# Kernel tuning notes

Measured on AMD Instinct MI355X. Metric: run time of the kernel, lower is better.

Reference implementation:

```python
import jax, jax.numpy as jnp
import numpy as np

NUM_CLASSES = 2
THRESHOLD = 0.35   # overlap_thresh
NEG_POS = 7        # negative:positive mining ratio
VAR0, VAR1 = 0.1, 0.2  # self.variance


def point_form(boxes):
    # (cx,cy,w,h) -> (xmin,ymin,xmax,ymax); boxes [P,4]
    return jnp.concatenate([boxes[:, :2] - boxes[:, 2:] / 2,
                            boxes[:, :2] + boxes[:, 2:] / 2], axis=1)


def jaccard(box_a, box_b):
    # box_a [B,O,4] xyxy, box_b [P,4] xyxy -> IoU [B,O,P]
    max_xy = jnp.minimum(box_a[:, :, None, 2:], box_b[None, None, :, 2:])
    min_xy = jnp.maximum(box_a[:, :, None, :2], box_b[None, None, :, :2])
    wh = jnp.clip(max_xy - min_xy, 0.0)
    inter = wh[..., 0] * wh[..., 1]
    area_a = ((box_a[..., 2] - box_a[..., 0]) * (box_a[..., 3] - box_a[..., 1]))[:, :, None]
    area_b = ((box_b[:, 2] - box_b[:, 0]) * (box_b[:, 3] - box_b[:, 1]))[None, None, :]
    return inter / (area_a + area_b - inter)


def encode(matched, priors):
    # matched [B,P,4] xyxy, priors [1,P,4] cxcywh -> offsets [B,P,4]
    g_cxcy = (matched[..., :2] + matched[..., 2:]) / 2 - priors[..., :2]
    g_cxcy = g_cxcy / (VAR0 * priors[..., 2:])
    g_wh = (matched[..., 2:] - matched[..., :2]) / priors[..., 2:]
    g_wh = jnp.log(g_wh) / VAR1
    return jnp.concatenate([g_cxcy, g_wh], axis=-1)


def match(truths, labels, priors):
    # truths [B,O,4] xyxy, labels [B,O] float, priors [P,4] cxcywh
    overlaps = jaccard(truths, point_form(priors))      # [B,O,P]
    best_prior_idx = jnp.argmax(overlaps, axis=2)       # [B,O] best prior per gt
    best_truth_overlap = jnp.max(overlaps, axis=1)      # [B,P]
    best_truth_idx = jnp.argmax(overlaps, axis=1)       # [B,P] best gt per prior
    O = truths.shape[1]

    def fix(bto, bti, bpi):
        # ensure every gt keeps its best prior (index_fill_ / loop in torch)
        bto = bto.at[bpi].set(2.0)
        bti = bti.at[bpi].set(jnp.arange(O))
        return bto, bti

    best_truth_overlap, best_truth_idx = jax.vmap(fix)(
        best_truth_overlap, best_truth_idx, best_prior_idx)
    matched = jnp.take_along_axis(truths, best_truth_idx[..., None], axis=1)  # [B,P,4]
    conf = jnp.take_along_axis(labels, best_truth_idx, axis=1).astype(jnp.int32) + 1
    conf = jnp.where(best_truth_overlap < THRESHOLD, 0, conf)  # background
    loc = encode(matched, priors[None])
    return loc, conf


def setup_inputs() -> dict:
    key = jax.random.key(0)
    k1, k2, k3, k4, k5, k6 = jax.random.split(key, 6)
    B, P, O, C = 32, 32768, 32, NUM_CLASSES
    loc_data = jax.random.normal(k1, (B, P, 4), jnp.float32)
    conf_data = jax.random.normal(k2, (B, P, C), jnp.float32)
    # priors: (cx,cy,w,h) in [0,1], wh in [0.02,0.3]
    p_cxcy = jax.random.uniform(k3, (P, 2), jnp.float32)
    p_wh = 0.02 + 0.28 * jax.random.uniform(k4, (P, 2), jnp.float32)
    priors = jnp.concatenate([p_cxcy, p_wh], axis=1)
    # targets: valid xyxy boxes + label column (label 0 -> class 1 after +1)
    t_cxcy = 0.1 + 0.8 * jax.random.uniform(k5, (B, O, 2), jnp.float32)
    t_wh = 0.05 + 0.2 * jax.random.uniform(k6, (B, O, 2), jnp.float32)
    boxes = jnp.concatenate([t_cxcy - t_wh / 2, t_cxcy + t_wh / 2], axis=2)
    labels = jnp.zeros((B, O, 1), jnp.float32)
    targets = jnp.concatenate([boxes, labels], axis=2)
    return {"loc_data": loc_data, "conf_data": conf_data,
            "priors": priors, "targets": targets}


def reference(loc_data, conf_data, priors, targets):
    B, P, C = conf_data.shape
    truths = targets[..., :4]
    labels = targets[..., 4]
    loc_t, conf_t = match(truths, labels, priors)   # [B,P,4], [B,P] int
    pos = conf_t > 0                                # [B,P]

    # localization: smooth-L1 summed over positives
    diff = loc_data - loc_t
    ad = jnp.abs(diff)
    sl1 = jnp.where(ad < 1.0, 0.5 * diff * diff, ad - 0.5)
    loss_l = jnp.sum(sl1 * pos[..., None].astype(loc_data.dtype))

    # per-prior CE loss for hard-negative mining
    lse = jax.nn.logsumexp(conf_data, axis=2)                            # [B,P]
    picked = jnp.take_along_axis(conf_data, conf_t[..., None], axis=2)[..., 0]
    ce = lse - picked                                                    # [B,P]
    mine = jnp.where(pos, 0.0, ce)
    # double-argsort rank trick (descending)
    loss_idx = jnp.argsort(-mine, axis=1)
    idx_rank = jnp.argsort(loss_idx, axis=1)
    num_pos = jnp.sum(pos, axis=1, keepdims=True)                        # [B,1]
    num_neg = jnp.minimum(NEG_POS * num_pos, P - 1)
    neg = idx_rank < num_neg

    sel = pos | neg
    loss_c = jnp.sum(jnp.where(sel, ce, 0.0))

    N = jnp.maximum(jnp.sum(num_pos).astype(jnp.float32), 1.0)
    return loss_l / N, loss_c / N
```

## Files before the change

### kernel.cpp

```cpp
#include <hip/hip_runtime.h>
#include <stdint.h>

#define NB 32
#define NP 32768
#define NO 32
#define THRESH 0.35f
#define NT1 64

typedef unsigned long long u64;
typedef unsigned int u32;

__device__ __forceinline__ float iou_corners(float px1, float py1, float px2, float py2, float ab,
                                             float tx1, float ty1, float tx2, float ty2, float aa)
{
#pragma clang fp contract(off)
    float iw = fminf(tx2, px2) - fmaxf(tx1, px1);
    float ih = fminf(ty2, py2) - fmaxf(ty1, py1);
    iw = fmaxf(iw, 0.f); ih = fmaxf(ih, 0.f);
    float inter = iw * ih;
    return __fdividef(inter, aa + ab - inter);
}

__device__ __forceinline__ float smooth_l1_sum(float4 ld, float4 pr, float4 tt)
{
#pragma clang fp contract(off)
    float g0 = __fdividef((tt.x + tt.z) * 0.5f - pr.x, 0.1f * pr.z);
    float g1 = __fdividef((tt.y + tt.w) * 0.5f - pr.y, 0.1f * pr.w);
    float g2 = __logf(__fdividef(tt.z - tt.x, pr.z)) * 5.0f;
    float g3 = __logf(__fdividef(tt.w - tt.y, pr.w)) * 5.0f;
    float d0 = ld.x - g0, d1 = ld.y - g1, d2 = ld.z - g2, d3 = ld.w - g3;
    float a0 = fabsf(d0), a1 = fabsf(d1), a2 = fabsf(d2), a3 = fabsf(d3);
    return (a0 < 1.f ? 0.5f * d0 * d0 : a0 - 0.5f)
         + (a1 < 1.f ? 0.5f * d1 * d1 : a1 - 0.5f)
         + (a2 < 1.f ? 0.5f * d2 * d2 : a2 - 0.5f)
         + (a3 < 1.f ? 0.5f * d3 * d3 : a3 - 0.5f);
}

__device__ __forceinline__ float lse2(float c0, float c1)
{
#pragma clang fp contract(off)
    float mm = fmaxf(c0, c1), mn = fminf(c0, c1);
    return mm + __logf(1.f + __expf(mn - mm));
}

__global__ __launch_bounds__(256) void kern1(
        const float* __restrict__ loc, const float* __restrict__ conf,
        const float* __restrict__ priors, const float* __restrict__ targets,
        float* __restrict__ mine, u64* __restrict__ bpk_part,
        float* __restrict__ part_sl1, float* __restrict__ part_cep, int* __restrict__ part_np,
        float* __restrict__ sl_tot, float* __restrict__ c_tot,
        int* __restrict__ np_tot, int* __restrict__ done_cnt)
{
#pragma clang fp contract(off)
    __shared__ __align__(16) float4 tbc[NO];
    __shared__ float ta[NO], tlab[NO];
    __shared__ u64 keys[NO];
    __shared__ float rs0[4], rs1[4];
    __shared__ int rc[4];
    const int b = blockIdx.y, x = blockIdx.x, tid = threadIdx.x;
    if (b == 0 && x == 0 && tid == 0) {
        *sl_tot = 0.f; *c_tot = 0.f; *np_tot = 0; *done_cnt = 0;
    }
    if (tid < NO * 5) {
        int o = tid / 5, c = tid % 5;
        float v = targets[b * NO * 5 + tid];
        if (c < 4) ((float*)&tbc[o])[c] = v; else tlab[o] = v;
    }
    if (tid < NO) keys[tid] = 0ull;
    __syncthreads();
    if (tid < NO) {
        float4 t = tbc[tid];
        ta[tid] = (t.z - t.x) * (t.w - t.y);
    }
    __syncthreads();

    const int p0 = x * 512 + tid * 2;
    float4 pr[2];
    float px1[2], py1[2], px2[2], py2[2], ab[2];
#pragma unroll
    for (int j = 0; j < 2; ++j) {
        pr[j] = ((const float4*)priors)[p0 + j];
        px1[j] = pr[j].x - pr[j].z * 0.5f;
        py1[j] = pr[j].y - pr[j].w * 0.5f;
        px2[j] = pr[j].x + pr[j].z * 0.5f;
        py2[j] = pr[j].y + pr[j].w * 0.5f;
        ab[j]  = pr[j].z * pr[j].w;
    }
    u64 bk[2] = {0ull, 0ull};
    const int lane_o = tid & 31;
    for (int it = 0; it < NO; ++it) {
        const int o = (it + lane_o) & 31;
        float4 tt = tbc[o];
        float aa = ta[o];
        float iou2[2];
#pragma unroll
        for (int j = 0; j < 2; ++j) {
            float iou = iou_corners(px1[j], py1[j], px2[j], py2[j], ab[j],
                                    tt.x, tt.y, tt.z, tt.w, aa);
            iou2[j] = iou;
            u64 ko = ((u64)__float_as_uint(iou) << 6) | (u64)(63 - o);
            bk[j] = bk[j] > ko ? bk[j] : ko;
        }
        float vm = fmaxf(iou2[0], iou2[1]);
        u64 cur = keys[o];
        if (__float_as_uint(vm) > (u32)(cur >> 32)) {
            float bi = iou2[1]; int bp = p0 + 1;
            if (iou2[0] >= bi) { bi = iou2[0]; bp = p0; }
            atomicMax(&keys[o], ((u64)__float_as_uint(bi) << 32) | (u64)(~(u32)bp));
        }
    }

    const size_t gbase = (size_t)b * NP + p0;
    float4 cf = ((const float4*)conf)[gbase >> 1];
    float c0[2] = {cf.x, cf.z};
    float c1[2] = {cf.y, cf.w};
    float2 mout;
    float s_sl1 = 0.f, s_cep = 0.f;
    int np = 0;
#pragma unroll
    for (int j = 0; j < 2; ++j) {
        u32 vb = (u32)(bk[j] >> 6);
        float bv = __uint_as_float(vb);
        int o = 63 - (int)(bk[j] & 63);
        int cfv = (bv < THRESH) ? 0 : ((int)tlab[o] + 1);
        bool pos = cfv > 0;
        float4 ld = ((const float4*)loc)[gbase + j];
        float sl1 = smooth_l1_sum(ld, pr[j], tbc[o]);
        float ce = lse2(c0[j], c1[j]) - ((cfv == 0) ? c0[j] : c1[j]);
        if (pos) { s_sl1 += sl1; s_cep += ce; np++; }
        ((float*)&mout)[j] = pos ? 0.f : ce;
    }
    ((float2*)mine)[gbase >> 1] = mout;

#pragma unroll
    for (int m = 32; m; m >>= 1) {
        s_sl1 += __shfl_xor(s_sl1, m, 64);
        s_cep += __shfl_xor(s_cep, m, 64);
        np    += __shfl_xor(np, m, 64);
    }
    int lane = tid & 63, w = tid >> 6;
    if (lane == 0) { rs0[w] = s_sl1; rs1[w] = s_cep; rc[w] = np; }
    __syncthreads();
    if (tid == 0) {
        float t0 = 0.f, t1 = 0.f; int t2 = 0;
        for (int i = 0; i < 4; ++i) { t0 += rs0[i]; t1 += rs1[i]; t2 += rc[i]; }
        part_sl1[b * NT1 + x] = t0;
        part_cep[b * NT1 + x] = t1;
        part_np [b * NT1 + x] = t2;
    }
    if (tid < NO) bpk_part[(b * NT1 + x) * 32 + tid] = keys[tid];
}

#define HCOL 33
__global__ __launch_bounds__(1024) void kern3(
        const float* __restrict__ loc, const float* __restrict__ conf,
        const float* __restrict__ priors, const float* __restrict__ targets,
        const u64* __restrict__ bpk_part, const float* __restrict__ mine,
        const float* __restrict__ part_sl1, const float* __restrict__ part_cep,
        const int* __restrict__ part_np,
        float* __restrict__ sl_tot, float* __restrict__ c_tot,
        int* __restrict__ np_tot, int* __restrict__ done_cnt,
        float* __restrict__ out)
{
#pragma clang fp contract(off)
    const int b = blockIdx.x, tid = threadIdx.x;
    const int wave = tid >> 6, lane = tid & 63;
    const int cl = lane & 31;
    __shared__ __align__(16) float4 tbc[NO];
    __shared__ float tlab[NO], tas[NO];
    __shared__ u32 pp[NO];
    __shared__ u32 flags[1024];
    __shared__ int hist[256 * HCOL];
    __shared__ int total[256];
    __shared__ float rs[16];
    __shared__ int rc2[16];
    __shared__ float sh_sl1, sh_cep;
    __shared__ int sh_np, sh_k, sh_kk;
    __shared__ u32 sh_prefix;

    if (tid < NO * 5) {
        int o = tid / 5, c = tid % 5;
        float v = targets[b * NO * 5 + tid];
        if (c < 4) ((float*)&tbc[o])[c] = v; else tlab[o] = v;
    }
    flags[tid] = 0u;
    for (int i = tid; i < 256 * HCOL; i += 1024) hist[i] = 0;

    const float* mb = mine + (size_t)b * NP;
    float v[32];
#pragma unroll
    for (int q = 0; q < 8; ++q) {
        float4 t4 = ((const float4*)mb)[q * 1024 + tid];
        v[4 * q] = t4.x; v[4 * q + 1] = t4.y; v[4 * q + 2] = t4.z; v[4 * q + 3] = t4.w;
    }
    __syncthreads();
#pragma unroll 8
    for (int j = 0; j < 32; ++j)
        atomicAdd(&hist[(__float_as_uint(v[j]) >> 24) * HCOL + cl], 1);
    if (tid < NO) {
        float4 t = tbc[tid];
        tas[tid] = (t.z - t.x) * (t.w - t.y);
        u64 key = 0ull;
        for (int xx = 0; xx < NT1; ++xx) {
            u64 t2 = bpk_part[(b * NT1 + xx) * 32 + tid];
            key = t2 > key ? t2 : key;
        }
        pp[tid] = (key >> 32) ? ~(u32)key : 0u;
    }
    __syncthreads();
    if (tid < NO) {
        const int o = tid;
        const u32 p = pp[o];
        float dsl1 = 0.f, dcep = 0.f; int dnp = 0;
        bool last = true;
        for (int o2 = o + 1; o2 < NO; ++o2)
            if (pp[o2] == p) { last = false; break; }
        if (last) {
            float4 prr = ((const float4*)priors)[p];
            float px1 = prr.x - prr.z * 0.5f, py1 = prr.y - prr.w * 0.5f;
            float px2 = prr.x + prr.z * 0.5f, py2 = prr.y + prr.w * 0.5f;
            float ab = prr.z * prr.w;
            float bv = -1.f; int bo_ = 0;
            for (int o2 = 0; o2 < NO; ++o2) {
                float4 t2 = tbc[o2];
                float i2 = iou_corners(px1, py1, px2, py2, ab, t2.x, t2.y, t2.z, t2.w, tas[o2]);
                if (i2 > bv) { bv = i2; bo_ = o2; }
            }
            int cf_pre = (bv < THRESH) ? 0 : ((int)tlab[bo_] + 1);
            size_t gp = (size_t)b * NP + p;
            float4 ld = ((const float4*)loc)[gp];
            float2 c = ((const float2*)conf)[gp];
            float lse = lse2(c.x, c.y);
            int cf_new = (int)tlab[o] + 1;
            dsl1 = smooth_l1_sum(ld, prr, tbc[o]);
            dcep = lse - ((cf_new == 0) ? c.x : c.y);
            dnp = 1;
            if (cf_pre > 0) {
                dsl1 -= smooth_l1_sum(ld, prr, tbc[bo_]);
                dcep -= lse - ((cf_pre == 0) ? c.x : c.y);
                dnp = 0;
            }
            float oldv = mb[p];
            atomicSub(&hist[(__float_as_uint(oldv) >> 24) * HCOL + cl], 1);
            atomicAdd(&hist[cl], 1);
            atomicOr(&flags[p >> 5], 1u << (p & 31));
        }
        float a = part_sl1[b * NT1 + o] + part_sl1[b * NT1 + 32 + o] + dsl1;
        float d = part_cep[b * NT1 + o] + part_cep[b * NT1 + 32 + o] + dcep;
        int   n = part_np [b * NT1 + o] + part_np [b * NT1 + 32 + o] + dnp;
#pragma unroll
        for (int m = 16; m; m >>= 1) {
            a += __shfl_xor(a, m, 32);
            d += __shfl_xor(d, m, 32);
            n += __shfl_xor(n, m, 32);
        }
        if (o == 0) {
            sh_sl1 = a; sh_cep = d; sh_np = n;
            sh_k = min(7 * n, NP - 1); sh_kk = sh_k; sh_prefix = 0u;
        }
    }
    __syncthreads();
#pragma unroll
    for (int q = 0; q < 8; ++q) {
        u32 word = flags[q * 128 + (tid >> 3)];
#pragma unroll
        for (int c = 0; c < 4; ++c)
            if ((word >> (((tid & 7) << 2) + c)) & 1u) v[4 * q + c] = 0.f;
    }
    const int k = sh_k;
    float topk = 0.f;
    if (k > 0) {
        for (int pass = 0; pass < 4; ++pass) {
            if (pass > 0) {
                for (int i = tid; i < 256 * HCOL; i += 1024) hist[i] = 0;
                __syncthreads();
                const int shift = 24 - 8 * pass;
                const u32 pfx = sh_prefix;
#pragma unroll 8
                for (int j = 0; j < 32; ++j) {
                    u32 kb = __float_as_uint(v[j]);
                    if ((u32)(((u64)kb) >> (shift + 8)) == pfx)
                        atomicAdd(&hist[((kb >> shift) & 255) * HCOL + cl], 1);
                }
                __syncthreads();
            }
            if (tid < 512) {
                int bin = tid >> 1;
                const int base = bin * HCOL + (tid & 1) * 16;
                int s = 0;
#pragma unroll
                for (int i = 0; i < 16; ++i) s += hist[base + i];
                s += __shfl_xor(s, 1, 64);
                if ((tid & 1) == 0) total[bin] = s;
            }
            __syncthreads();
            if (tid < 64) {
                int4 h4 = ((const int4*)total)[tid];
                int s3 = h4.w, s2 = h4.z + s3, s1 = h4.y + s2, s0 = h4.x + s1;
                int acc = s0;
#pragma unroll
                for (int off = 1; off < 64; off <<= 1) {
                    int u = __shfl_down(acc, off, 64);
                    if (tid + off < 64) acc += u;
                }
                int excl = acc - s0;
                int kk = sh_kk;
                int cand = -1, nkk = 0;
                if (excl + s3 >= kk)      { cand = 4 * tid + 3; nkk = kk - excl; }
                else if (excl + s2 >= kk) { cand = 4 * tid + 2; nkk = kk - excl - s3; }
                else if (excl + s1 >= kk) { cand = 4 * tid + 1; nkk = kk - excl - s2; }
                else if (excl + s0 >= kk) { cand = 4 * tid + 0; nkk = kk - excl - s1; }
                int cmax = cand;
#pragma unroll
                for (int off = 1; off < 64; off <<= 1) cmax = max(cmax, __shfl_xor(cmax, off, 64));
                if (cand >= 0 && cand == cmax) {
                    sh_prefix = (sh_prefix << 8) | (u32)(cand & 255);
                    sh_kk = nkk;
                }
            }
            __syncthreads();
        }
        const u32 T = sh_prefix;
        const float tval = __uint_as_float(T);
        float s = 0.f; int c2 = 0;
#pragma unroll
        for (int j = 0; j < 32; ++j) {
            if (__float_as_uint(v[j]) > T) { s += v[j]; c2++; }
        }
#pragma unroll
        for (int m = 32; m; m >>= 1) {
            s  += __shfl_xor(s, m, 64);
            c2 += __shfl_xor(c2, m, 64);
        }
        if (lane == 0) { rs[wave] = s; rc2[wave] = c2; }
        __syncthreads();
        if (tid == 0) {
            float st = 0.f; int ct = 0;
            for (int i = 0; i < 16; ++i) { st += rs[i]; ct += rc2[i]; }
            topk = st + (float)(k - ct) * tval;
        }
    }
    if (tid == 0) {
        atomicAdd(sl_tot, sh_sl1);
        atomicAdd(c_tot, sh_cep + topk);
        atomicAdd(np_tot, sh_np);
        __threadfence();
        int d = atomicAdd(done_cnt, 1);
        if (d == NB - 1) {
            float sl = atomicAdd(sl_tot, 0.f);
            float cc = atomicAdd(c_tot, 0.f);
            int   np = atomicAdd(np_tot, 0);
            float N = fmaxf((float)np, 1.f);
            out[0] = sl / N;
            out[1] = cc / N;
        }
    }
}

extern "C" void kernel_launch(void* const* d_in, const int* in_sizes, int n_in,
                              void* d_out, int out_size, void* d_ws, size_t ws_size,
                              hipStream_t stream) {
    const float* loc     = (const float*)d_in[0];
    const float* conf    = (const float*)d_in[1];
    const float* priors  = (const float*)d_in[2];
    const float* targets = (const float*)d_in[3];
    float* out = (float*)d_out;

    char* ws = (char*)d_ws;
    float* mine     = (float*)ws;
    u64*   bpk_part = (u64*)(ws + 4194304);
    float* part_sl1 = (float*)(ws + 4718592);
    float* part_cep = (float*)(ws + 4726784);
    int*   part_np  = (int*)(ws + 4734976);
    float* sl_tot   = (float*)(ws + 4743168);
    float* c_tot    = (float*)(ws + 4743172);
    int*   np_tot   = (int*)(ws + 4743176);
    int*   done_cnt = (int*)(ws + 4743180);

    dim3 g1(NT1, NB);
    kern1<<<g1, 256, 0, stream>>>(loc, conf, priors, targets, mine, bpk_part,
                                  part_sl1, part_cep, part_np,
                                  sl_tot, c_tot, np_tot, done_cnt);
    kern3<<<NB, 1024, 0, stream>>>(loc, conf, priors, targets, bpk_part, mine,
                                   part_sl1, part_cep, part_np,
                                   sl_tot, c_tot, np_tot, done_cnt, out);
}
```

Measured before the change: 127.4 us.

## Replace 4-pass 8-bit radix select with 3-pass 13/13/6-bit histogram select

The per-batch top-k threshold search used four 8-bit radix passes over replicated 256x33 histograms. It now uses three passes with wider digits (13, 13 and 6 bits) over plain 8192-bin shared histograms, found with a block-wide suffix scan. This cuts the number of passes and block barriers. In exchange, the single-copy histograms suffer more atomic contention, and each scan now reads more bins.

```diff
diff --git a/kernel.cpp b/kernel.cpp
--- a/kernel.cpp
+++ b/kernel.cpp
@@ -6,6 +6,7 @@
 #define NO 32
 #define THRESH 0.35f
 #define NT1 64
+#define HB 8192
 
 typedef unsigned long long u64;
 typedef unsigned int u32;
@@ -151,7 +152,6 @@
     if (tid < NO) bpk_part[(b * NT1 + x) * 32 + tid] = keys[tid];
 }
 
-#define HCOL 33
 __global__ __launch_bounds__(1024) void kern3(
         const float* __restrict__ loc, const float* __restrict__ conf,
         const float* __restrict__ priors, const float* __restrict__ targets,
@@ -165,18 +165,18 @@
 #pragma clang fp contract(off)
     const int b = blockIdx.x, tid = threadIdx.x;
     const int wave = tid >> 6, lane = tid & 63;
-    const int cl = lane & 31;
     __shared__ __align__(16) float4 tbc[NO];
     __shared__ float tlab[NO], tas[NO];
     __shared__ u32 pp[NO];
     __shared__ u32 flags[1024];
-    __shared__ int hist[256 * HCOL];
-    __shared__ int total[256];
+    __shared__ int histA[HB], histB[HB];
+    __shared__ int wtot[16];
     __shared__ float rs[16];
     __shared__ int rc2[16];
     __shared__ float sh_sl1, sh_cep;
-    __shared__ int sh_np, sh_k, sh_kk;
-    __shared__ u32 sh_prefix;
+    __shared__ int sh_np, sh_k, sh_kk0, sh_kk1, sh_kk2;
+    __shared__ int sh_pA, sh_pB;
+    __shared__ u32 sh_T;
 
     if (tid < NO * 5) {
         int o = tid / 5, c = tid % 5;
@@ -184,8 +184,11 @@
         if (c < 4) ((float*)&tbc[o])[c] = v; else tlab[o] = v;
     }
     flags[tid] = 0u;
-    for (int i = tid; i < 256 * HCOL; i += 1024) hist[i] = 0;
-
+#pragma unroll
+    for (int i = 0; i < HB / 1024; ++i) {
+        histA[tid + 1024 * i] = 0;
+        histB[tid + 1024 * i] = 0;
+    }
     const float* mb = mine + (size_t)b * NP;
     float v[32];
 #pragma unroll
@@ -194,9 +197,10 @@
         v[4 * q] = t4.x; v[4 * q + 1] = t4.y; v[4 * q + 2] = t4.z; v[4 * q + 3] = t4.w;
     }
     __syncthreads();
+
 #pragma unroll 8
     for (int j = 0; j < 32; ++j)
-        atomicAdd(&hist[(__float_as_uint(v[j]) >> 24) * HCOL + cl], 1);
+        atomicAdd(&histA[__float_as_uint(v[j]) >> 19], 1);
     if (tid < NO) {
         float4 t = tbc[tid];
         tas[tid] = (t.z - t.x) * (t.w - t.y);
@@ -208,6 +212,7 @@
         pp[tid] = (key >> 32) ? ~(u32)key : 0u;
     }
     __syncthreads();
+
     if (tid < NO) {
         const int o = tid;
         const u32 p = pp[o];
@@ -241,8 +246,8 @@
                 dnp = 0;
             }
             float oldv = mb[p];
-            atomicSub(&hist[(__float_as_uint(oldv) >> 24) * HCOL + cl], 1);
-            atomicAdd(&hist[cl], 1);
+            atomicSub(&histA[__float_as_uint(oldv) >> 19], 1);
+            atomicAdd(&histA[0], 1);
             atomicOr(&flags[p >> 5], 1u << (p & 31));
         }
         float a = part_sl1[b * NT1 + o] + part_sl1[b * NT1 + 32 + o] + dsl1;
@@ -256,83 +261,116 @@
         }
         if (o == 0) {
             sh_sl1 = a; sh_cep = d; sh_np = n;
-            sh_k = min(7 * n, NP - 1); sh_kk = sh_k; sh_prefix = 0u;
-        }
-    }
-    __syncthreads();
-#pragma unroll
-    for (int q = 0; q < 8; ++q) {
-        u32 word = flags[q * 128 + (tid >> 3)];
-#pragma unroll
-        for (int c = 0; c < 4; ++c)
-            if ((word >> (((tid & 7) << 2) + c)) & 1u) v[4 * q + c] = 0.f;
-    }
+            sh_k = min(7 * n, NP - 1); sh_kk0 = sh_k;
+        }
+    }
+    __syncthreads();
+
     const int k = sh_k;
+    const int base = tid << 3;
     float topk = 0.f;
     if (k > 0) {
-        for (int pass = 0; pass < 4; ++pass) {
-            if (pass > 0) {
-                for (int i = tid; i < 256 * HCOL; i += 1024) hist[i] = 0;
-                __syncthreads();
-                const int shift = 24 - 8 * pass;
-                const u32 pfx = sh_prefix;
-#pragma unroll 8
-                for (int j = 0; j < 32; ++j) {
-                    u32 kb = __float_as_uint(v[j]);
-                    if ((u32)(((u64)kb) >> (shift + 8)) == pfx)
-                        atomicAdd(&hist[((kb >> shift) & 255) * HCOL + cl], 1);
-                }
-                __syncthreads();
-            }
-            if (tid < 512) {
-                int bin = tid >> 1;
-                const int base = bin * HCOL + (tid & 1) * 16;
-                int s = 0;
-#pragma unroll
-                for (int i = 0; i < 16; ++i) s += hist[base + i];
-                s += __shfl_xor(s, 1, 64);
-                if ((tid & 1) == 0) total[bin] = s;
-            }
-            __syncthreads();
-            if (tid < 64) {
-                int4 h4 = ((const int4*)total)[tid];
-                int s3 = h4.w, s2 = h4.z + s3, s1 = h4.y + s2, s0 = h4.x + s1;
-                int acc = s0;
-#pragma unroll
-                for (int off = 1; off < 64; off <<= 1) {
-                    int u = __shfl_down(acc, off, 64);
-                    if (tid + off < 64) acc += u;
-                }
-                int excl = acc - s0;
-                int kk = sh_kk;
-                int cand = -1, nkk = 0;
-                if (excl + s3 >= kk)      { cand = 4 * tid + 3; nkk = kk - excl; }
-                else if (excl + s2 >= kk) { cand = 4 * tid + 2; nkk = kk - excl - s3; }
-                else if (excl + s1 >= kk) { cand = 4 * tid + 1; nkk = kk - excl - s2; }
-                else if (excl + s0 >= kk) { cand = 4 * tid + 0; nkk = kk - excl - s1; }
-                int cmax = cand;
-#pragma unroll
-                for (int off = 1; off < 64; off <<= 1) cmax = max(cmax, __shfl_xor(cmax, off, 64));
-                if (cand >= 0 && cand == cmax) {
-                    sh_prefix = (sh_prefix << 8) | (u32)(cand & 255);
-                    sh_kk = nkk;
+#pragma unroll
+        for (int q = 0; q < 8; ++q) {
+            u32 word = flags[q * 128 + (tid >> 3)];
+#pragma unroll
+            for (int c = 0; c < 4; ++c)
+                if ((word >> (((tid & 7) << 2) + c)) & 1u) v[4 * q + c] = 0.f;
+        }
+        int s = 0;
+#pragma unroll
+        for (int i = 0; i < 8; ++i)
+            s += histA[base + ((i + tid) & 7)];
+        int suf = s;
+#pragma unroll
+        for (int off = 1; off < 64; off <<= 1) {
+            int u = __shfl_down(suf, off, 64);
+            if (lane + off < 64) suf += u;
+        }
+        if (lane == 0) wtot[wave] = suf;
+        __syncthreads();
+        {
+            int excl = suf - s;
+            for (int w = wave + 1; w < 16; ++w) excl += wtot[w];
+            int kk = sh_kk0;
+            if (excl < kk && kk <= excl + s) {
+                int c = excl;
+                for (int j = 7; j >= 0; --j) {
+                    int cnt = histA[base + j];
+                    if (kk <= c + cnt) { sh_pA = base + j; sh_kk1 = kk - c; break; }
+                    c += cnt;
                 }
             }
-            __syncthreads();
-        }
-        const u32 T = sh_prefix;
+        }
+        __syncthreads();
+        const u32 pA = (u32)sh_pA;
+        if (tid < 64) histA[tid] = 0;
+#pragma unroll 8
+        for (int j = 0; j < 32; ++j) {
+            u32 kb = __float_as_uint(v[j]);
+            if ((kb >> 19) == pA) atomicAdd(&histB[(kb >> 6) & (HB - 1)], 1);
+        }
+        __syncthreads();
+        int s2 = 0;
+#pragma unroll
+        for (int i = 0; i < 8; ++i)
+            s2 += histB[base + ((i + tid) & 7)];
+        int suf2 = s2;
+#pragma unroll
+        for (int off = 1; off < 64; off <<= 1) {
+            int u = __shfl_down(suf2, off, 64);
+            if (lane + off < 64) suf2 += u;
+        }
+        if (lane == 0) wtot[wave] = suf2;
+        __syncthreads();
+        {
+            int excl = suf2 - s2;
+            for (int w = wave + 1; w < 16; ++w) excl += wtot[w];
+            int kk = sh_kk1;
+            if (excl < kk && kk <= excl + s2) {
+                int c = excl;
+                for (int j = 7; j >= 0; --j) {
+                    int cnt = histB[base + j];
+                    if (kk <= c + cnt) { sh_pB = base + j; sh_kk2 = kk - c; break; }
+                    c += cnt;
+                }
+            }
+        }
+        __syncthreads();
+        const u32 p26 = (pA << 13) | (u32)sh_pB;
+#pragma unroll 8
+        for (int j = 0; j < 32; ++j) {
+            u32 kb = __float_as_uint(v[j]);
+            if ((kb >> 6) == p26) atomicAdd(&histA[kb & 63], 1);
+        }
+        __syncthreads();
+        if (tid < 64) {
+            int s3 = histA[tid];
+            int suf3 = s3;
+#pragma unroll
+            for (int off = 1; off < 64; off <<= 1) {
+                int u = __shfl_down(suf3, off, 64);
+                if (tid + off < 64) suf3 += u;
+            }
+            int excl = suf3 - s3;
+            int kk = sh_kk2;
+            if (excl < kk && kk <= excl + s3)
+                sh_T = ((u32)sh_pA << 19) | ((u32)sh_pB << 6) | (u32)tid;
+        }
+        __syncthreads();
+        const u32 T = sh_T;
         const float tval = __uint_as_float(T);
-        float s = 0.f; int c2 = 0;
+        float ssum = 0.f; int c2 = 0;
 #pragma unroll
         for (int j = 0; j < 32; ++j) {
-            if (__float_as_uint(v[j]) > T) { s += v[j]; c2++; }
+            if (__float_as_uint(v[j]) > T) { ssum += v[j]; c2++; }
         }
 #pragma unroll
         for (int m = 32; m; m >>= 1) {
-            s  += __shfl_xor(s, m, 64);
-            c2 += __shfl_xor(c2, m, 64);
-        }
-        if (lane == 0) { rs[wave] = s; rc2[wave] = c2; }
+            ssum += __shfl_xor(ssum, m, 64);
+            c2   += __shfl_xor(c2, m, 64);
+        }
+        if (lane == 0) { rs[wave] = ssum; rc2[wave] = c2; }
         __syncthreads();
         if (tid == 0) {
             float st = 0.f; int ct = 0;
```

After: 135.8 us. +6.6%, slower.
